# Kernel optimization log

Hardware: AMD Instinct MI355X
Metric: run time of the kernel (lower is better)

The kernel has to match this reference:

```python
import jax, jax.numpy as jnp
import numpy as np

N_NODES = 100000


def gcn_conv(x, edge_index, W, b):
    """PyG GCNConv: add self-loops, symmetric deg^-1/2 normalization, linear."""
    n = x.shape[0]
    h = x @ W  # [N, out]
    loop = jnp.arange(n, dtype=edge_index.dtype)
    src = jnp.concatenate([edge_index[0], loop])
    dst = jnp.concatenate([edge_index[1], loop])
    deg = jax.ops.segment_sum(jnp.ones_like(dst, dtype=h.dtype), dst, num_segments=n)
    dinv = jnp.where(deg > 0, jax.lax.rsqrt(deg), 0.0)
    norm = dinv[src] * dinv[dst]  # [E+N]
    msg = h[src] * norm[:, None]  # gather + scale
    out = jax.ops.segment_sum(msg, dst, num_segments=n)  # scatter-add
    return out + b


def setup_inputs() -> dict:
    key = jax.random.key(0)
    k1, k2, k3, k4 = jax.random.split(key, 4)
    d_in, d_hid, d_out = 128, 128, 128  # output_dim // 2 = 128
    E = 1600000
    x = jax.random.normal(k1, (N_NODES, d_in), dtype=jnp.float32)
    edge_index = jax.random.randint(k2, (2, E), 0, N_NODES, dtype=jnp.int64)
    s1 = 1.0 / np.sqrt(d_in)
    s2 = 1.0 / np.sqrt(d_hid)
    W1 = jax.random.normal(k3, (d_in, d_hid), dtype=jnp.float32) * s1
    b1 = jnp.zeros((d_hid,), dtype=jnp.float32)
    W2 = jax.random.normal(k4, (d_hid, d_out), dtype=jnp.float32) * s2
    b2 = jnp.zeros((d_out,), dtype=jnp.float32)
    return {"x": x, "edge_index": edge_index, "W1": W1, "b1": b1, "W2": W2, "b2": b2}


def reference(x, edge_index, W1, b1, W2, b2):
    h = jax.nn.relu(gcn_conv(x, edge_index, W1, b1))
    # dropout(p=0.5) is identity in eval mode
    return gcn_conv(h, edge_index, W2, b2)
```

## Files before the change

kernel.cpp:

```cpp
#include <hip/hip_runtime.h>

#define D 128

typedef unsigned int uint;
typedef unsigned short ushort;
typedef __attribute__((ext_vector_type(8))) short bf16x8_t;
typedef __attribute__((ext_vector_type(4))) float f32x4_t;

#define BSH 9
#define BMASK 511
#define BN 512
#define CAP 9216
#define CHUNK 2048
#define NBUCKP 256

__device__ inline uint bf16rn(float f) {
    uint u = __float_as_uint(f);
    return (u + 0x7fffu + ((u >> 16) & 1u)) >> 16;
}

__global__ __launch_bounds__(256) void kp_scatter3(const int* __restrict__ src,
                                                   const int* __restrict__ dst,
                                                   int* __restrict__ gcnt,
                                                   uint* __restrict__ bkt, int E, int nbuck) {
    __shared__ uint stage[CHUNK];
    __shared__ int cnt[NBUCKP], loc[NBUCKP], gbase[NBUCKP];
    int t = threadIdx.x;
    int base = blockIdx.x * CHUNK;
    int end = min(E, base + CHUNK);

    cnt[t] = 0; gbase[t] = 0;
    __syncthreads();
    uint pk[8]; int bk[8]; int rk[8];
#pragma unroll
    for (int it = 0; it < 8; it++) {
        int i = base + t + it * 256;
        if (i < end) {
            int d = dst[i], s = src[i];
            bk[it] = d >> BSH;
            pk[it] = ((uint)s << BSH) | (uint)(d & BMASK);
            rk[it] = atomicAdd(&cnt[bk[it]], 1);
        } else {
            bk[it] = 0; pk[it] = 0u; rk[it] = -1;
        }
    }
    __syncthreads();
    int v = cnt[t];
    loc[t] = v;
    __syncthreads();
    for (int off = 1; off < NBUCKP; off <<= 1) {
        int x = (t >= off) ? loc[t - off] : 0;
        __syncthreads();
        loc[t] += x;
        __syncthreads();
    }
    if (t < nbuck && cnt[t] > 0)
        gbase[t] = atomicAdd(&gcnt[t], cnt[t]);
    __syncthreads();
#pragma unroll
    for (int it = 0; it < 8; it++)
        if (rk[it] >= 0)
            stage[(loc[bk[it]] - cnt[bk[it]]) + rk[it]] = pk[it];
    __syncthreads();
    int grp = t >> 4, gl = t & 15;
    for (int b2 = grp; b2 < nbuck; b2 += 16) {
        int c = cnt[b2];
        if (c == 0) continue;
        int lo = loc[b2] - c;
        int gb = gbase[b2];
        uint* ob = bkt + (size_t)b2 * CAP;
        for (int j = gl; j < c; j += 16) {
            int di = gb + j;
            if (di < CAP) ob[di] = stage[lo + j];
        }
    }
}

__global__ __launch_bounds__(512) void kp_build3(uint* __restrict__ bkt,
                                                 const int* __restrict__ gcnt,
                                                 int2* __restrict__ row_se,
                                                 float* __restrict__ dinv, int n, int nbuck,
                                                 const float* __restrict__ W1,
                                                 const float* __restrict__ W2,
                                                 ushort* __restrict__ W1h, ushort* __restrict__ W1l,
                                                 ushort* __restrict__ W2h, ushort* __restrict__ W2l) {
    int t = threadIdx.x, b = blockIdx.x;
    if (b >= nbuck) {
        int i = (b - nbuck) * 512 + t;
        int sel = i >> 14;
        int j = i & 16383;
        int k = j >> 7, nn = j & 127;
        const float* W = sel ? W2 : W1;
        float w = W[k * D + nn];
        uint hb = bf16rn(w);
        float hf = __uint_as_float(hb << 16);
        uint lb = bf16rn(w - hf);
        if (sel) { W2h[nn * D + k] = (ushort)hb; W2l[nn * D + k] = (ushort)lb; }
        else     { W1h[nn * D + k] = (ushort)hb; W1l[nn * D + k] = (ushort)lb; }
        return;
    }
    __shared__ uint ents[CAP];
    __shared__ ushort ranks[CAP];
    __shared__ int cnt[BN], loc[BN];
    int m = gcnt[b];
    if (m > CAP) m = CAP;
    uint* bk = bkt + (size_t)b * CAP;
    for (int i = t; i < m; i += 512) ents[i] = bk[i];
    cnt[t] = 0;
    __syncthreads();
    for (int i = t; i < m; i += 512) {
        int r = atomicAdd(&cnt[ents[i] & BMASK], 1);
        ranks[i] = (ushort)r;
    }
    __syncthreads();
    int v = cnt[t];
    loc[t] = v;
    __syncthreads();
    for (int off = 1; off < BN; off <<= 1) {
        int x = (t >= off) ? loc[t - off] : 0;
        __syncthreads();
        loc[t] += x;
        __syncthreads();
    }
    int base = b * CAP;
    int node = (b << BSH) + t;
    if (node < n) {
        row_se[node] = make_int2(base + loc[t] - v, base + loc[t]);
        dinv[node] = rsqrtf((float)(v + 1));
    }
    __syncthreads();
    for (int i = t; i < m; i += 512) {
        uint p = ents[i];
        int low = p & BMASK;
        ((int*)bk)[(loc[low] - cnt[low]) + (int)ranks[i]] = (int)((p >> BSH) << 8);
    }
}

__device__ inline void accum_bf16x8(float* a, uint4 v) {
    a[0] += __uint_as_float(v.x << 16);
    a[1] += __uint_as_float(v.x & 0xffff0000u);
    a[2] += __uint_as_float(v.y << 16);
    a[3] += __uint_as_float(v.y & 0xffff0000u);
    a[4] += __uint_as_float(v.z << 16);
    a[5] += __uint_as_float(v.z & 0xffff0000u);
    a[6] += __uint_as_float(v.w << 16);
    a[7] += __uint_as_float(v.w & 0xffff0000u);
}

template <bool A_FP32>
__global__ __launch_bounds__(512, 4) void k_gemm_mfma(const void* __restrict__ A,
                                                      const ushort* __restrict__ Wth,
                                                      const ushort* __restrict__ Wtl,
                                                      const float* __restrict__ dinv,
                                                      ushort* __restrict__ Yb, int M) {
    constexpr int STR = 36;
    constexpr int TILE = 128 * STR;
    __shared__ ushort lds[A_FP32 ? 4 * TILE : 3 * TILE];
    ushort* Ah = lds;
    ushort* Wh = lds + TILE;
    ushort* Wl = lds + 2 * TILE;
    ushort* Al = A_FP32 ? (lds + 3 * TILE) : nullptr;

    int t = threadIdx.x;
    int lane = t & 63, wave = t >> 6;
    int quad = lane >> 4, l16 = lane & 15;
    int m_off = (wave >> 2) * 64;
    int n_off = (wave & 3) * 32;
    int block_row = blockIdx.x * 128;

    f32x4_t acc[4][2];
#pragma unroll
    for (int mt = 0; mt < 4; mt++)
#pragma unroll
        for (int nt = 0; nt < 2; nt++) acc[mt][nt] = (f32x4_t){0.f, 0.f, 0.f, 0.f};

    for (int kc = 0; kc < 128; kc += 32) {
        if (A_FP32) {
            const float* Af = (const float*)A;
#pragma unroll
            for (int it = 0; it < 2; it++) {
                int s = t + it * 512;
                int row = s >> 3, kl = (s & 7) * 4;
                int gr = block_row + row;
                float4 v = make_float4(0.f, 0.f, 0.f, 0.f);
                if (gr < M) v = *(const float4*)(Af + (size_t)gr * D + kc + kl);
                ushort4 h, l;
                uint hb, lb; float hf;
                hb = bf16rn(v.x); hf = __uint_as_float(hb << 16); lb = bf16rn(v.x - hf);
                h.x = (ushort)hb; l.x = (ushort)lb;
                hb = bf16rn(v.y); hf = __uint_as_float(hb << 16); lb = bf16rn(v.y - hf);
                h.y = (ushort)hb; l.y = (ushort)lb;
                hb = bf16rn(v.z); hf = __uint_as_float(hb << 16); lb = bf16rn(v.z - hf);
                h.z = (ushort)hb; l.z = (ushort)lb;
                hb = bf16rn(v.w); hf = __uint_as_float(hb << 16); lb = bf16rn(v.w - hf);
                h.w = (ushort)hb; l.w = (ushort)lb;
                *(ushort4*)&Ah[row * STR + kl] = h;
                *(ushort4*)&Al[row * STR + kl] = l;
            }
        } else {
            const ushort* Ab = (const ushort*)A;
            {
                int s = t;
                int row = s >> 2, kl = (s & 3) * 8;
                int gr = block_row + row;
                uint4 v = make_uint4(0u, 0u, 0u, 0u);
                if (gr < M) v = *(const uint4*)(Ab + (size_t)gr * D + kc + kl);
                *(uint4*)&Ah[row * STR + kl] = v;
            }
        }
        {
            int s = t;
            int nrow = s >> 2, kl = (s & 3) * 8;
            *(uint4*)&Wh[nrow * STR + kl] = *(const uint4*)(Wth + nrow * D + kc + kl);
            *(uint4*)&Wl[nrow * STR + kl] = *(const uint4*)(Wtl + nrow * D + kc + kl);
        }
        __syncthreads();

        {
            int kf = quad * 8;
            bf16x8_t ah[4], bh[2], bl[2];
#pragma unroll
            for (int mt = 0; mt < 4; mt++)
                ah[mt] = *(const bf16x8_t*)&Ah[(m_off + mt * 16 + l16) * STR + kf];
#pragma unroll
            for (int nt = 0; nt < 2; nt++) {
                bh[nt] = *(const bf16x8_t*)&Wh[(n_off + nt * 16 + l16) * STR + kf];
                bl[nt] = *(const bf16x8_t*)&Wl[(n_off + nt * 16 + l16) * STR + kf];
            }
            if (A_FP32) {
                bf16x8_t al[4];
#pragma unroll
                for (int mt = 0; mt < 4; mt++)
                    al[mt] = *(const bf16x8_t*)&Al[(m_off + mt * 16 + l16) * STR + kf];
#pragma unroll
                for (int mt = 0; mt < 4; mt++)
#pragma unroll
                    for (int nt = 0; nt < 2; nt++) {
                        acc[mt][nt] = __builtin_amdgcn_mfma_f32_16x16x32_bf16(ah[mt], bh[nt], acc[mt][nt], 0, 0, 0);
                        acc[mt][nt] = __builtin_amdgcn_mfma_f32_16x16x32_bf16(al[mt], bh[nt], acc[mt][nt], 0, 0, 0);
                        acc[mt][nt] = __builtin_amdgcn_mfma_f32_16x16x32_bf16(ah[mt], bl[nt], acc[mt][nt], 0, 0, 0);
                    }
            } else {
#pragma unroll
                for (int mt = 0; mt < 4; mt++)
#pragma unroll
                    for (int nt = 0; nt < 2; nt++) {
                        acc[mt][nt] = __builtin_amdgcn_mfma_f32_16x16x32_bf16(ah[mt], bh[nt], acc[mt][nt], 0, 0, 0);
                        acc[mt][nt] = __builtin_amdgcn_mfma_f32_16x16x32_bf16(ah[mt], bl[nt], acc[mt][nt], 0, 0, 0);
                    }
            }
        }
        __syncthreads();
    }

#pragma unroll
    for (int mt = 0; mt < 4; mt++) {
#pragma unroll
        for (int reg = 0; reg < 4; reg++) {
            int gr = block_row + m_off + mt * 16 + quad * 4 + reg;
            if (gr < M) {
                float di = dinv[gr];
#pragma unroll
                for (int nt = 0; nt < 2; nt++) {
                    int colg = n_off + nt * 16 + l16;
                    Yb[(size_t)gr * D + colg] = (ushort)bf16rn(di * acc[mt][nt][reg]);
                }
            }
        }
    }
}

__global__ __launch_bounds__(256) void k_agg(const ushort* __restrict__ Hb,
                                             const int2* __restrict__ row_se,
                                             const int* __restrict__ colb,
                                             const float* __restrict__ dinv,
                                             const float* __restrict__ bias,
                                             float* __restrict__ Yf, ushort* __restrict__ Yb,
                                             int n, int do_relu, int out_bf16) {
    __shared__ int ls[4][64];
    int wv = threadIdx.x >> 6;
    int node = blockIdx.x * 4 + wv;
    int lane = threadIdx.x & 63;
    int chain = lane >> 4;
    int l16   = lane & 15;
    if (node >= n) return;

    int2 se = row_se[node];
    int start = se.x, end = se.y;

    float a0[8], a1[8];
#pragma unroll
    for (int k = 0; k < 8; k++) { a0[k] = 0.f; a1[k] = 0.f; }

    const char* hbase = (const char*)Hb;
    uint loff = (uint)l16 * 16u;

    if (chain == 0) {
        uint4 v = *(const uint4*)(hbase + (uint)node * 256u + loff);
        accum_bf16x8(a0, v);
    }

    for (int tb = start; tb < end; tb += 64) {
        int idx = tb + lane;
        ls[wv][lane] = (idx < end) ? colb[idx] : 0;
        int c = min(64, end - tb);
        int j = chain;
        for (; j + 12 < c; j += 16) {
            uint o0 = (uint)ls[wv][j];
            uint o1 = (uint)ls[wv][j + 4];
            uint o2 = (uint)ls[wv][j + 8];
            uint o3 = (uint)ls[wv][j + 12];
            uint4 v0 = *(const uint4*)(hbase + o0 + loff);
            uint4 v1 = *(const uint4*)(hbase + o1 + loff);
            uint4 v2 = *(const uint4*)(hbase + o2 + loff);
            uint4 v3 = *(const uint4*)(hbase + o3 + loff);
            accum_bf16x8(a0, v0);
            accum_bf16x8(a1, v1);
            accum_bf16x8(a0, v2);
            accum_bf16x8(a1, v3);
        }
        for (; j + 4 < c; j += 8) {
            uint o0 = (uint)ls[wv][j];
            uint o1 = (uint)ls[wv][j + 4];
            uint4 v0 = *(const uint4*)(hbase + o0 + loff);
            uint4 v1 = *(const uint4*)(hbase + o1 + loff);
            accum_bf16x8(a0, v0);
            accum_bf16x8(a1, v1);
        }
        if (j < c) {
            uint o0 = (uint)ls[wv][j];
            uint4 v0 = *(const uint4*)(hbase + o0 + loff);
            accum_bf16x8(a0, v0);
        }
    }

    float acc[8];
#pragma unroll
    for (int k = 0; k < 8; k++) {
        float v = a0[k] + a1[k];
        v += __shfl_xor(v, 16, 64);
        v += __shfl_xor(v, 32, 64);
        acc[k] = v;
    }

    if (chain == 0) {
        float di = dinv[node];
        const float4* bp = (const float4*)bias + l16 * 2;
        float4 b0 = bp[0], b1 = bp[1];
        float o[8];
        o[0] = fmaf(di, acc[0], b0.x); o[1] = fmaf(di, acc[1], b0.y);
        o[2] = fmaf(di, acc[2], b0.z); o[3] = fmaf(di, acc[3], b0.w);
        o[4] = fmaf(di, acc[4], b1.x); o[5] = fmaf(di, acc[5], b1.y);
        o[6] = fmaf(di, acc[6], b1.z); o[7] = fmaf(di, acc[7], b1.w);
        if (do_relu) {
#pragma unroll
            for (int k = 0; k < 8; k++) o[k] = fmaxf(o[k], 0.f);
        }
        if (out_bf16) {
            uint4 pk;
            pk.x = bf16rn(o[0]) | (bf16rn(o[1]) << 16);
            pk.y = bf16rn(o[2]) | (bf16rn(o[3]) << 16);
            pk.z = bf16rn(o[4]) | (bf16rn(o[5]) << 16);
            pk.w = bf16rn(o[6]) | (bf16rn(o[7]) << 16);
            ((uint4*)(Yb + (size_t)node * D))[l16] = pk;
        } else {
            f32x4_t q0 = {o[0], o[1], o[2], o[3]};
            f32x4_t q1 = {o[4], o[5], o[6], o[7]};
            f32x4_t* yp = (f32x4_t*)(Yf + (size_t)node * D) + l16 * 2;
            __builtin_nontemporal_store(q0, yp);
            __builtin_nontemporal_store(q1, yp + 1);
        }
    }
}

extern "C" void kernel_launch(void* const* d_in, const int* in_sizes, int n_in,
                              void* d_out, int out_size, void* d_ws, size_t ws_size,
                              hipStream_t stream) {
    const float* x  = (const float*)d_in[0];
    const int*   ei = (const int*)d_in[1];
    const float* W1 = (const float*)d_in[2];
    const float* b1 = (const float*)d_in[3];
    const float* W2 = (const float*)d_in[4];
    const float* b2 = (const float*)d_in[5];
    float* out = (float*)d_out;

    int n = in_sizes[0] / D;
    int E = in_sizes[1] / 2;
    const int* src = ei;
    const int* dst = ei + E;

    int nbuck = (n + BMASK) >> BSH;

    char* p = (char*)d_ws;
    ushort* h_buf = (ushort*)p; p += (size_t)n * D * sizeof(ushort);
    ushort* y_buf = (ushort*)p; p += (size_t)n * D * sizeof(ushort);
    ushort* w1h   = (ushort*)p; p += (size_t)D * D * sizeof(ushort);
    ushort* w1l   = (ushort*)p; p += (size_t)D * D * sizeof(ushort);
    ushort* w2h   = (ushort*)p; p += (size_t)D * D * sizeof(ushort);
    ushort* w2l   = (ushort*)p; p += (size_t)D * D * sizeof(ushort);
    uint*  bkt    = (uint*)p;   p += (size_t)nbuck * CAP * sizeof(uint);
    float* dinv   = (float*)p;  p += (size_t)n * sizeof(float);
    int2*  row_se = (int2*)p;   p += (size_t)n * sizeof(int2);
    int*   gcnt   = (int*)p;    p += (size_t)nbuck * sizeof(int);

    (void)hipMemsetAsync(gcnt, 0, (size_t)nbuck * sizeof(int), stream);
    int sc_grid = (E + CHUNK - 1) / CHUNK;
    kp_scatter3<<<sc_grid, 256, 0, stream>>>(src, dst, gcnt, bkt, E, nbuck);
    kp_build3<<<nbuck + 64, 512, 0, stream>>>(bkt, gcnt, row_se, dinv, n, nbuck,
                                              W1, W2, w1h, w1l, w2h, w2l);

    int gemm_grid = (n + 127) / 128;
    int agg_grid  = (n + 3) / 4;
    const int* colp = (const int*)bkt;

    k_gemm_mfma<true><<<gemm_grid, 512, 0, stream>>>(x, w1h, w1l, dinv, h_buf, n);
    k_agg<<<agg_grid, 256, 0, stream>>>(h_buf, row_se, colp, dinv, b1, nullptr, y_buf, n, 1, 1);
    k_gemm_mfma<false><<<gemm_grid, 512, 0, stream>>>(y_buf, w2h, w2l, dinv, h_buf, n);
    k_agg<<<agg_grid, 256, 0, stream>>>(h_buf, row_se, colp, dinv, b2, out, nullptr, n, 0, 0);
}
```

Before: 371.1 us.

## Keep full weight tile in LDS and load A fragments directly from global memory

The GEMM kernel now loads the whole split-bf16 weight matrix (hi and lo) into LDS once per block. Each wave reads its A operand fragments straight from global memory into registers, splitting fp32 to hi/lo in registers instead of staging through LDS. This removes the per-k-chunk LDS staging and the two barriers per iteration. Blocks shrink to 256 threads with 64x64 wave tiles (16 accumulators per wave). The cost is higher register pressure and uncoalesced row-strided global reads of A.

```diff
diff --git a/kernel.cpp b/kernel.cpp
--- a/kernel.cpp
+++ b/kernel.cpp
@@ -147,110 +147,99 @@
     a[7] += __uint_as_float(v.w & 0xffff0000u);
 }
 
+__device__ inline void split8(float4 v0, float4 v1, bf16x8_t* hh, bf16x8_t* ll) {
+    float f[8] = {v0.x, v0.y, v0.z, v0.w, v1.x, v1.y, v1.z, v1.w};
+    bf16x8_t h, l;
+#pragma unroll
+    for (int i = 0; i < 8; i++) {
+        uint hb = bf16rn(f[i]);
+        float hf = __uint_as_float(hb << 16);
+        uint lb = bf16rn(f[i] - hf);
+        h[i] = (short)hb;
+        l[i] = (short)lb;
+    }
+    *hh = h; *ll = l;
+}
+
 template <bool A_FP32>
-__global__ __launch_bounds__(512, 4) void k_gemm_mfma(const void* __restrict__ A,
+__global__ __launch_bounds__(256, 2) void k_gemm_mfma(const void* __restrict__ A,
                                                       const ushort* __restrict__ Wth,
                                                       const ushort* __restrict__ Wtl,
                                                       const float* __restrict__ dinv,
                                                       ushort* __restrict__ Yb, int M) {
-    constexpr int STR = 36;
-    constexpr int TILE = 128 * STR;
-    __shared__ ushort lds[A_FP32 ? 4 * TILE : 3 * TILE];
-    ushort* Ah = lds;
-    ushort* Wh = lds + TILE;
-    ushort* Wl = lds + 2 * TILE;
-    ushort* Al = A_FP32 ? (lds + 3 * TILE) : nullptr;
+    constexpr int STR = 136;
+    __shared__ ushort Wh[128 * STR];
+    __shared__ ushort Wl[128 * STR];
 
     int t = threadIdx.x;
     int lane = t & 63, wave = t >> 6;
     int quad = lane >> 4, l16 = lane & 15;
-    int m_off = (wave >> 2) * 64;
-    int n_off = (wave & 3) * 32;
+    int m_off = (wave >> 1) * 64;
+    int n_off = (wave & 1) * 64;
     int block_row = blockIdx.x * 128;
 
-    f32x4_t acc[4][2];
+#pragma unroll
+    for (int it = 0; it < 8; it++) {
+        int s = t + it * 256;
+        int nrow = s >> 4, kl = (s & 15) * 8;
+        *(uint4*)&Wh[nrow * STR + kl] = *(const uint4*)(Wth + nrow * D + kl);
+        *(uint4*)&Wl[nrow * STR + kl] = *(const uint4*)(Wtl + nrow * D + kl);
+    }
+    __syncthreads();
+
+    f32x4_t acc[4][4];
 #pragma unroll
     for (int mt = 0; mt < 4; mt++)
 #pragma unroll
-        for (int nt = 0; nt < 2; nt++) acc[mt][nt] = (f32x4_t){0.f, 0.f, 0.f, 0.f};
-
-    for (int kc = 0; kc < 128; kc += 32) {
+        for (int nt = 0; nt < 4; nt++) acc[mt][nt] = (f32x4_t){0.f, 0.f, 0.f, 0.f};
+
+    const bf16x8_t zf = (bf16x8_t){0, 0, 0, 0, 0, 0, 0, 0};
+
+#pragma unroll 2
+    for (int ks = 0; ks < 4; ks++) {
+        int kc = ks * 32 + quad * 8;
+        bf16x8_t ah[4], al[4];
         if (A_FP32) {
             const float* Af = (const float*)A;
 #pragma unroll
-            for (int it = 0; it < 2; it++) {
-                int s = t + it * 512;
-                int row = s >> 3, kl = (s & 7) * 4;
-                int gr = block_row + row;
-                float4 v = make_float4(0.f, 0.f, 0.f, 0.f);
-                if (gr < M) v = *(const float4*)(Af + (size_t)gr * D + kc + kl);
-                ushort4 h, l;
-                uint hb, lb; float hf;
-                hb = bf16rn(v.x); hf = __uint_as_float(hb << 16); lb = bf16rn(v.x - hf);
-                h.x = (ushort)hb; l.x = (ushort)lb;
-                hb = bf16rn(v.y); hf = __uint_as_float(hb << 16); lb = bf16rn(v.y - hf);
-                h.y = (ushort)hb; l.y = (ushort)lb;
-                hb = bf16rn(v.z); hf = __uint_as_float(hb << 16); lb = bf16rn(v.z - hf);
-                h.z = (ushort)hb; l.z = (ushort)lb;
-                hb = bf16rn(v.w); hf = __uint_as_float(hb << 16); lb = bf16rn(v.w - hf);
-                h.w = (ushort)hb; l.w = (ushort)lb;
-                *(ushort4*)&Ah[row * STR + kl] = h;
-                *(ushort4*)&Al[row * STR + kl] = l;
+            for (int mt = 0; mt < 4; mt++) {
+                int gr = block_row + m_off + mt * 16 + l16;
+                float4 v0 = make_float4(0.f, 0.f, 0.f, 0.f);
+                float4 v1 = make_float4(0.f, 0.f, 0.f, 0.f);
+                if (gr < M) {
+                    const float* rp = Af + (size_t)gr * D + kc;
+                    v0 = *(const float4*)rp;
+                    v1 = *(const float4*)(rp + 4);
+                }
+                split8(v0, v1, &ah[mt], &al[mt]);
             }
         } else {
             const ushort* Ab = (const ushort*)A;
-            {
-                int s = t;
-                int row = s >> 2, kl = (s & 3) * 8;
-                int gr = block_row + row;
-                uint4 v = make_uint4(0u, 0u, 0u, 0u);
-                if (gr < M) v = *(const uint4*)(Ab + (size_t)gr * D + kc + kl);
-                *(uint4*)&Ah[row * STR + kl] = v;
+#pragma unroll
+            for (int mt = 0; mt < 4; mt++) {
+                int gr = block_row + m_off + mt * 16 + l16;
+                ah[mt] = (gr < M) ? *(const bf16x8_t*)(Ab + (size_t)gr * D + kc) : zf;
             }
         }
-        {
-            int s = t;
-            int nrow = s >> 2, kl = (s & 3) * 8;
-            *(uint4*)&Wh[nrow * STR + kl] = *(const uint4*)(Wth + nrow * D + kc + kl);
-            *(uint4*)&Wl[nrow * STR + kl] = *(const uint4*)(Wtl + nrow * D + kc + kl);
-        }
-        __syncthreads();
-
-        {
-            int kf = quad * 8;
-            bf16x8_t ah[4], bh[2], bl[2];
-#pragma unroll
-            for (int mt = 0; mt < 4; mt++)
-                ah[mt] = *(const bf16x8_t*)&Ah[(m_off + mt * 16 + l16) * STR + kf];
-#pragma unroll
-            for (int nt = 0; nt < 2; nt++) {
-                bh[nt] = *(const bf16x8_t*)&Wh[(n_off + nt * 16 + l16) * STR + kf];
-                bl[nt] = *(const bf16x8_t*)&Wl[(n_off + nt * 16 + l16) * STR + kf];
+#pragma unroll
+        for (int nt = 0; nt < 4; nt++) {
+            bf16x8_t bh = *(const bf16x8_t*)&Wh[(n_off + nt * 16 + l16) * STR + kc];
+            bf16x8_t bl = *(const bf16x8_t*)&Wl[(n_off + nt * 16 + l16) * STR + kc];
+            if (A_FP32) {
+#pragma unroll
+                for (int mt = 0; mt < 4; mt++) {
+                    acc[mt][nt] = __builtin_amdgcn_mfma_f32_16x16x32_bf16(ah[mt], bh, acc[mt][nt], 0, 0, 0);
+                    acc[mt][nt] = __builtin_amdgcn_mfma_f32_16x16x32_bf16(al[mt], bh, acc[mt][nt], 0, 0, 0);
+                    acc[mt][nt] = __builtin_amdgcn_mfma_f32_16x16x32_bf16(ah[mt], bl, acc[mt][nt], 0, 0, 0);
+                }
+            } else {
+#pragma unroll
+                for (int mt = 0; mt < 4; mt++) {
+                    acc[mt][nt] = __builtin_amdgcn_mfma_f32_16x16x32_bf16(ah[mt], bh, acc[mt][nt], 0, 0, 0);
+                    acc[mt][nt] = __builtin_amdgcn_mfma_f32_16x16x32_bf16(ah[mt], bl, acc[mt][nt], 0, 0, 0);
+                }
             }
-            if (A_FP32) {
-                bf16x8_t al[4];
-#pragma unroll
-                for (int mt = 0; mt < 4; mt++)
-                    al[mt] = *(const bf16x8_t*)&Al[(m_off + mt * 16 + l16) * STR + kf];
-#pragma unroll
-                for (int mt = 0; mt < 4; mt++)
-#pragma unroll
-                    for (int nt = 0; nt < 2; nt++) {
-                        acc[mt][nt] = __builtin_amdgcn_mfma_f32_16x16x32_bf16(ah[mt], bh[nt], acc[mt][nt], 0, 0, 0);
-                        acc[mt][nt] = __builtin_amdgcn_mfma_f32_16x16x32_bf16(al[mt], bh[nt], acc[mt][nt], 0, 0, 0);
-                        acc[mt][nt] = __builtin_amdgcn_mfma_f32_16x16x32_bf16(ah[mt], bl[nt], acc[mt][nt], 0, 0, 0);
-                    }
-            } else {
-#pragma unroll
-                for (int mt = 0; mt < 4; mt++)
-#pragma unroll
-                    for (int nt = 0; nt < 2; nt++) {
-                        acc[mt][nt] = __builtin_amdgcn_mfma_f32_16x16x32_bf16(ah[mt], bh[nt], acc[mt][nt], 0, 0, 0);
-                        acc[mt][nt] = __builtin_amdgcn_mfma_f32_16x16x32_bf16(ah[mt], bl[nt], acc[mt][nt], 0, 0, 0);
-                    }
-            }
-        }
-        __syncthreads();
+        }
     }
 
 #pragma unroll
@@ -261,7 +250,7 @@
             if (gr < M) {
                 float di = dinv[gr];
 #pragma unroll
-                for (int nt = 0; nt < 2; nt++) {
+                for (int nt = 0; nt < 4; nt++) {
                     int colg = n_off + nt * 16 + l16;
                     Yb[(size_t)gr * D + colg] = (ushort)bf16rn(di * acc[mt][nt][reg]);
                 }
@@ -413,8 +402,8 @@
     int agg_grid  = (n + 3) / 4;
     const int* colp = (const int*)bkt;
 
-    k_gemm_mfma<true><<<gemm_grid, 512, 0, stream>>>(x, w1h, w1l, dinv, h_buf, n);
+    k_gemm_mfma<true><<<gemm_grid, 256, 0, stream>>>(x, w1h, w1l, dinv, h_buf, n);
     k_agg<<<agg_grid, 256, 0, stream>>>(h_buf, row_se, colp, dinv, b1, nullptr, y_buf, n, 1, 1);
-    k_gemm_mfma<false><<<gemm_grid, 512, 0, stream>>>(y_buf, w2h, w2l, dinv, h_buf, n);
+    k_gemm_mfma<false><<<gemm_grid, 256, 0, stream>>>(y_buf, w2h, w2l, dinv, h_buf, n);
     k_agg<<<agg_grid, 256, 0, stream>>>(h_buf, row_se, colp, dinv, b2, out, nullptr, n, 0, 0);
 }
```

Result: faster. 314.2 us (-15.3%).
